# Performance work log

Measured on AMD Instinct MI355X. Metric: run time of the kernel, lower is better.

Reference implementation:

```python
import jax, jax.numpy as jnp
import numpy as np

B, S, DIN, DOUT = 2, 2048, 4096, 4096


def setup_inputs() -> dict:
    key = jax.random.key(0)
    k1, k2, k3, k4, k5 = jax.random.split(key, 5)
    x = jax.random.normal(k1, (B, S, DIN), dtype=jnp.float32)
    # int8-range weights stored as int32 (faithful to q_int_weight.float() upcast)
    q_int_weight = jax.random.randint(k2, (DIN, DOUT), 0, 256, dtype=jnp.int32)
    scale = jax.random.uniform(k3, (1,), dtype=jnp.float32) * 0.01 + 0.001
    zero_point = jax.random.uniform(k4, (1,), dtype=jnp.float32) * 128.0
    bias = jax.random.normal(k5, (DOUT,), dtype=jnp.float32)
    return {"x": x, "q_int_weight": q_int_weight, "scale": scale,
            "zero_point": zero_point, "bias": bias}


def reference(x, q_int_weight, scale, zero_point, bias):
    # Dequantize: (q - zero_point) * scale, per-tensor affine. Stored [in, out].
    w = (q_int_weight.astype(jnp.float32) - zero_point) * scale  # [DIN, DOUT]
    # F.linear(x_flat, w.t(), bias) == x @ w + bias
    y = jnp.einsum('bsi,io->bso', x, w) + bias  # [B, S, DOUT]
    return y
```

## Files before the change

### kernel.cpp

```cpp
#include <hip/hip_runtime.h>
#include <cstdint>
#include <cstddef>

#define M_DIM 4096
#define N_DIM 4096
#define K_DIM 4096
#define BM 128
#define BN 128
#define BKB 128

typedef __attribute__((ext_vector_type(4))) int i32x4;

__device__ __forceinline__ void async_copy16(const void* g, void* l) {
  __builtin_amdgcn_global_load_lds(
      (const __attribute__((address_space(1))) void*)g,
      (__attribute__((address_space(3))) void*)l,
      16, 0, 0);
}

__global__ __launch_bounds__(256) void convert_x_kernel(
    const float* __restrict__ x, signed char* __restrict__ xi,
    float* __restrict__ sx, float* __restrict__ rs) {
  __shared__ float red[8];
  const int t = threadIdx.x;
  const size_t row = blockIdx.x;
  const float* xr = x + row * (size_t)K_DIM;

  float4 v[4];
  float amax = 0.f;
#pragma unroll
  for (int i = 0; i < 4; ++i) {
    v[i] = *(const float4*)(xr + (i * 256 + t) * 4);
    amax = fmaxf(amax, fmaxf(fmaxf(fabsf(v[i].x), fabsf(v[i].y)),
                             fmaxf(fabsf(v[i].z), fabsf(v[i].w))));
  }
#pragma unroll
  for (int o = 32; o > 0; o >>= 1)
    amax = fmaxf(amax, __shfl_down(amax, o, 64));
  if ((t & 63) == 0) red[t >> 6] = amax;
  __syncthreads();
  amax = fmaxf(fmaxf(fmaxf(red[0], red[1]), fmaxf(red[2], red[3])), 1e-20f);
  const float inv = 127.f / amax;

  int ssum = 0;
  signed char* out = xi + row * (size_t)K_DIM;
#pragma unroll
  for (int i = 0; i < 4; ++i) {
    const int ia = __float2int_rn(v[i].x * inv);
    const int ib = __float2int_rn(v[i].y * inv);
    const int ic = __float2int_rn(v[i].z * inv);
    const int id = __float2int_rn(v[i].w * inv);
    ssum += ia + ib + ic + id;
    const int pk =
        (ia & 255) | ((ib & 255) << 8) | ((ic & 255) << 16) | (id << 24);
    *(int*)(out + (i * 256 + t) * 4) = pk;
  }
  float fs = (float)ssum;
#pragma unroll
  for (int o = 32; o > 0; o >>= 1) fs += __shfl_down(fs, o, 64);
  if ((t & 63) == 0) red[4 + (t >> 6)] = fs;
  __syncthreads();
  if (t == 0) {
    rs[row] = red[4] + red[5] + red[6] + red[7];
    sx[row] = amax * (1.f / 127.f);
  }
}

__global__ __launch_bounds__(256) void convert_w_kernel(
    const int* __restrict__ q, signed char* __restrict__ qsT) {
  __shared__ __align__(16) int qtile[64][68];
  const int t = threadIdx.x;
  const int k0 = (blockIdx.x & 63) << 6;
  const int n0 = (blockIdx.x >> 6) << 6;

  {
    const int c = t & 15;
    const int r0 = t >> 4;
#pragma unroll
    for (int i = 0; i < 4; ++i) {
      const int r = r0 + i * 16;
      const int4 v = *(const int4*)(q + (size_t)(k0 + r) * N_DIM + n0 + c * 4);
      *(int4*)&qtile[r][c * 4] = v;
    }
  }
  __syncthreads();
  {
    const int kc = t & 15;
    const int g = t >> 4;
    int4 v[4];
#pragma unroll
    for (int i = 0; i < 4; ++i) v[i] = *(const int4*)&qtile[kc * 4 + i][g * 4];
#pragma unroll
    for (int j = 0; j < 4; ++j) {
      const int b0 = ((&v[0].x)[j] - 128) & 255;
      const int b1 = ((&v[1].x)[j] - 128) & 255;
      const int b2 = ((&v[2].x)[j] - 128) & 255;
      const int b3 = ((&v[3].x)[j] - 128) & 255;
      const int pk = b0 | (b1 << 8) | (b2 << 16) | (b3 << 24);
      *(int*)(qsT + (size_t)(n0 + g * 4 + j) * K_DIM + k0 + kc * 4) = pk;
    }
  }
}

__global__ __launch_bounds__(256) void gemm_kernel(
    const signed char* __restrict__ A,
    const signed char* __restrict__ Bt,
    const float* __restrict__ bias, const float* __restrict__ sx,
    const float* __restrict__ rs, const float* __restrict__ scale_p,
    const float* __restrict__ zp_p, float* __restrict__ C) {
  __shared__ __align__(16) signed char As[BM * BKB];
  __shared__ __align__(16) signed char Bs[BN * BKB];

  const int tid = threadIdx.x;
  const int wave = tid >> 6;
  const int lane = tid & 63;
  const int wm = wave & 1;
  const int wn = wave >> 1;

  const int bm = blockIdx.x & 31;
  const int bn = blockIdx.x >> 5;
  const size_t m0 = (size_t)bm * BM;
  const size_t n0 = (size_t)bn * BN;

  const int srow = lane >> 3;
  const int schunk = (lane & 7) ^ (lane >> 3);

  const int quad = lane >> 4;
  const int lrow = lane & 15;
  const int rsw = lrow & 7;

  i32x4 acc[4][4];
  const i32x4 zero = {0, 0, 0, 0};
#pragma unroll
  for (int i = 0; i < 4; ++i)
#pragma unroll
    for (int j = 0; j < 4; ++j) acc[i][j] = zero;

  const signed char* Abase = A + m0 * K_DIM;
  const signed char* Bbase = Bt + n0 * K_DIM;

  for (int k0 = 0; k0 < K_DIM; k0 += BKB) {
#pragma unroll
    for (int j = 0; j < 4; ++j) {
      const int rbase = wave * 32 + j * 8;
      const int row = rbase + srow;
      const size_t goff = (size_t)row * K_DIM + k0 + schunk * 16;
      async_copy16(Abase + goff, As + rbase * BKB);
      async_copy16(Bbase + goff, Bs + rbase * BKB);
    }
    __syncthreads();

#pragma unroll
    for (int kh = 0; kh < 2; ++kh) {
      i32x4 af[4], bfr[4];
#pragma unroll
      for (int t = 0; t < 4; ++t) {
        const int ar = wm * 64 + t * 16 + lrow;
        const int br = wn * 64 + t * 16 + lrow;
        const int ch = (kh * 4 + quad) ^ rsw;
        af[t] = *(const i32x4*)(As + ar * BKB + ch * 16);
        bfr[t] = *(const i32x4*)(Bs + br * BKB + ch * 16);
      }
#pragma unroll
      for (int i = 0; i < 4; ++i)
#pragma unroll
        for (int j = 0; j < 4; ++j)
          acc[i][j] = __builtin_amdgcn_mfma_i32_16x16x64_i8(
              af[i], bfr[j], acc[i][j], 0, 0, 0);
    }
    __syncthreads();
  }

  const float scale = scale_p[0];
  const float c1 = 128.f - zp_p[0];
  float am[4][4], bm_[4][4];
#pragma unroll
  for (int i = 0; i < 4; ++i) {
    const size_t mbase = m0 + wm * 64 + i * 16 + quad * 4;
#pragma unroll
    for (int r = 0; r < 4; ++r) {
      const float a = scale * sx[mbase + r];
      am[i][r] = a;
      bm_[i][r] = a * c1 * rs[mbase + r];
    }
  }
#pragma unroll
  for (int j = 0; j < 4; ++j) {
    const size_t n = n0 + wn * 64 + j * 16 + lrow;
    const float bv = bias[n];
#pragma unroll
    for (int i = 0; i < 4; ++i) {
      const size_t mbase = m0 + wm * 64 + i * 16 + quad * 4;
#pragma unroll
      for (int r = 0; r < 4; ++r) {
        C[(mbase + r) * N_DIM + n] =
            fmaf(am[i][r], (float)acc[i][j][r], bm_[i][r] + bv);
      }
    }
  }
}

extern "C" void kernel_launch(void* const* d_in, const int* in_sizes, int n_in,
                              void* d_out, int out_size, void* d_ws,
                              size_t ws_size, hipStream_t stream) {
  const float* x = (const float*)d_in[0];
  const int* q = (const int*)d_in[1];
  const float* scale = (const float*)d_in[2];
  const float* zp = (const float*)d_in[3];
  const float* bias = (const float*)d_in[4];
  float* out = (float*)d_out;

  char* ws = (char*)d_ws;
  signed char* xi = (signed char*)ws;
  signed char* qsT = (signed char*)(ws + ((size_t)16 << 20));
  float* sx = (float*)(ws + ((size_t)32 << 20));
  float* rs = (float*)(ws + ((size_t)32 << 20) + (16 << 10));

  convert_x_kernel<<<4096, 256, 0, stream>>>(x, xi, sx, rs);
  convert_w_kernel<<<4096, 256, 0, stream>>>(q, qsT);
  gemm_kernel<<<1024, 256, 0, stream>>>(xi, qsT, bias, sx, rs, scale, zp, out);
}
```

Measured before the change: 262.0 us.

## Use 256x256 double-buffered int8 GEMM tiles with interleaved LDS loads and MFMA

Grows the GEMM block tile to 256x256 with 8 waves and double-buffers the A and B tiles in LDS, so the next K tile is loaded while the current one is multiplied. LDS fragment reads and MFMA groups are interleaved across barriers, with s_setprio raising priority during the MFMA groups. Blocks are remapped in a swizzled order to improve L2 reuse. The larger tile cuts global traffic per MFMA, but it uses 128KB of LDS and many accumulator registers. That limits occupancy, and 256 blocks leave only one wave of work across the device.

```diff
diff --git a/kernel.cpp b/kernel.cpp
--- a/kernel.cpp
+++ b/kernel.cpp
@@ -5,9 +5,10 @@
 #define M_DIM 4096
 #define N_DIM 4096
 #define K_DIM 4096
-#define BM 128
-#define BN 128
+#define BM 256
+#define BN 256
 #define BKB 128
+#define KTILES (K_DIM / BKB)
 
 typedef __attribute__((ext_vector_type(4))) int i32x4;
 
@@ -102,99 +103,149 @@
   }
 }
 
-__global__ __launch_bounds__(256) void gemm_kernel(
+__global__ __launch_bounds__(512, 2) void gemm_kernel(
     const signed char* __restrict__ A,
     const signed char* __restrict__ Bt,
     const float* __restrict__ bias, const float* __restrict__ sx,
     const float* __restrict__ rs, const float* __restrict__ scale_p,
     const float* __restrict__ zp_p, float* __restrict__ C) {
-  __shared__ __align__(16) signed char As[BM * BKB];
-  __shared__ __align__(16) signed char Bs[BN * BKB];
+  __shared__ __align__(16) signed char As[2][BM * BKB];
+  __shared__ __align__(16) signed char Bs[2][BN * BKB];
 
   const int tid = threadIdx.x;
   const int wave = tid >> 6;
   const int lane = tid & 63;
-  const int wm = wave & 1;
-  const int wn = wave >> 1;
-
-  const int bm = blockIdx.x & 31;
-  const int bn = blockIdx.x >> 5;
+  const int wm = wave >> 2;
+  const int wn = wave & 3;
+
+  const int swz = (blockIdx.x & 7) * 32 + (blockIdx.x >> 3);
+  const int bm = swz & 15;
+  const int bn = swz >> 4;
   const size_t m0 = (size_t)bm * BM;
   const size_t n0 = (size_t)bn * BN;
 
   const int srow = lane >> 3;
-  const int schunk = (lane & 7) ^ (lane >> 3);
+  const int schunk = (lane & 7) ^ srow;
 
   const int quad = lane >> 4;
   const int lrow = lane & 15;
   const int rsw = lrow & 7;
 
-  i32x4 acc[4][4];
+  const signed char* Abase = A + m0 * K_DIM + schunk * 16;
+  const signed char* Bbase = Bt + n0 * K_DIM + schunk * 16;
+
+  i32x4 acc[8][4];
   const i32x4 zero = {0, 0, 0, 0};
 #pragma unroll
-  for (int i = 0; i < 4; ++i)
+  for (int i = 0; i < 8; ++i)
 #pragma unroll
     for (int j = 0; j < 4; ++j) acc[i][j] = zero;
 
-  const signed char* Abase = A + m0 * K_DIM;
-  const signed char* Bbase = Bt + n0 * K_DIM;
-
-  for (int k0 = 0; k0 < K_DIM; k0 += BKB) {
+  auto stage = [&](int b, int k0) {
 #pragma unroll
     for (int j = 0; j < 4; ++j) {
-      const int rbase = wave * 32 + j * 8;
-      const int row = rbase + srow;
-      const size_t goff = (size_t)row * K_DIM + k0 + schunk * 16;
-      async_copy16(Abase + goff, As + rbase * BKB);
-      async_copy16(Bbase + goff, Bs + rbase * BKB);
-    }
-    __syncthreads();
-
-#pragma unroll
-    for (int kh = 0; kh < 2; ++kh) {
-      i32x4 af[4], bfr[4];
-#pragma unroll
-      for (int t = 0; t < 4; ++t) {
-        const int ar = wm * 64 + t * 16 + lrow;
-        const int br = wn * 64 + t * 16 + lrow;
-        const int ch = (kh * 4 + quad) ^ rsw;
-        af[t] = *(const i32x4*)(As + ar * BKB + ch * 16);
-        bfr[t] = *(const i32x4*)(Bs + br * BKB + ch * 16);
-      }
-#pragma unroll
-      for (int i = 0; i < 4; ++i)
-#pragma unroll
-        for (int j = 0; j < 4; ++j)
-          acc[i][j] = __builtin_amdgcn_mfma_i32_16x16x64_i8(
-              af[i], bfr[j], acc[i][j], 0, 0, 0);
-    }
-    __syncthreads();
-  }
+      const int rbase = j * 64 + wave * 8;
+      const size_t go = (size_t)(rbase + srow) * K_DIM + k0;
+      async_copy16(Abase + go, (void*)&As[b][rbase * BKB]);
+      async_copy16(Bbase + go, (void*)&Bs[b][rbase * BKB]);
+    }
+  };
+
+#define LDA(ig)                                                              \
+  do {                                                                       \
+    _Pragma("unroll") for (int kh = 0; kh < 2; ++kh)                         \
+        _Pragma("unroll") for (int t = 0; t < 4; ++t) {                      \
+      const int ar = wm * 128 + (ig) * 64 + t * 16 + lrow;                   \
+      av[kh][t] =                                                            \
+          *(const i32x4*)(as + ar * BKB + ((((kh << 2) | quad) ^ rsw) << 4));\
+    }                                                                        \
+  } while (0)
+
+#define LDB(jg)                                                              \
+  do {                                                                       \
+    _Pragma("unroll") for (int kh = 0; kh < 2; ++kh)                         \
+        _Pragma("unroll") for (int t = 0; t < 2; ++t) {                      \
+      const int br = wn * 64 + ((jg) * 2 + t) * 16 + lrow;                   \
+      bv[kh][(jg) * 2 + t] =                                                 \
+          *(const i32x4*)(bs + br * BKB + ((((kh << 2) | quad) ^ rsw) << 4));\
+    }                                                                        \
+  } while (0)
+
+#define MFMA16(ibase, j0)                                                    \
+  do {                                                                       \
+    __builtin_amdgcn_s_setprio(1);                                           \
+    _Pragma("unroll") for (int kh = 0; kh < 2; ++kh)                         \
+        _Pragma("unroll") for (int t = 0; t < 4; ++t)                        \
+            _Pragma("unroll") for (int j = 0; j < 2; ++j)                    \
+        acc[(ibase) + t][(j0) + j] = __builtin_amdgcn_mfma_i32_16x16x64_i8(  \
+            av[kh][t], bv[kh][(j0) + j], acc[(ibase) + t][(j0) + j], 0, 0,   \
+            0);                                                              \
+    __builtin_amdgcn_s_setprio(0);                                           \
+  } while (0)
+
+  stage(0, 0);
+  asm volatile("s_waitcnt vmcnt(0)" ::: "memory");
+  __builtin_amdgcn_s_barrier();
+
+#pragma unroll 2
+  for (int kt = 0; kt < KTILES; ++kt) {
+    const int buf = kt & 1;
+    const signed char* as = As[buf];
+    const signed char* bs = Bs[buf];
+
+    if (kt + 1 < KTILES) stage(buf ^ 1, (kt + 1) * BKB);
+
+    i32x4 av[2][4], bv[2][4];
+
+    LDA(0);
+    LDB(0);
+    __builtin_amdgcn_s_barrier();
+    MFMA16(0, 0);
+    __builtin_amdgcn_s_barrier();
+
+    LDB(1);
+    __builtin_amdgcn_s_barrier();
+    MFMA16(0, 2);
+    __builtin_amdgcn_s_barrier();
+
+    LDA(1);
+    __builtin_amdgcn_s_barrier();
+    MFMA16(4, 2);
+    __builtin_amdgcn_s_barrier();
+
+    MFMA16(4, 0);
+
+    __builtin_amdgcn_sched_barrier(0);
+    asm volatile("s_waitcnt lgkmcnt(0)" ::: "memory");
+    asm volatile("s_waitcnt vmcnt(0)" ::: "memory");
+    __builtin_amdgcn_sched_barrier(0);
+    __builtin_amdgcn_s_barrier();
+  }
+
+#undef LDA
+#undef LDB
+#undef MFMA16
 
   const float scale = scale_p[0];
   const float c1 = 128.f - zp_p[0];
-  float am[4][4], bm_[4][4];
-#pragma unroll
-  for (int i = 0; i < 4; ++i) {
-    const size_t mbase = m0 + wm * 64 + i * 16 + quad * 4;
+#pragma unroll
+  for (int i = 0; i < 8; ++i) {
+    const size_t mbase = m0 + wm * 128 + i * 16 + quad * 4;
+    float am[4], bmv[4];
 #pragma unroll
     for (int r = 0; r < 4; ++r) {
       const float a = scale * sx[mbase + r];
-      am[i][r] = a;
-      bm_[i][r] = a * c1 * rs[mbase + r];
-    }
-  }
-#pragma unroll
-  for (int j = 0; j < 4; ++j) {
-    const size_t n = n0 + wn * 64 + j * 16 + lrow;
-    const float bv = bias[n];
-#pragma unroll
-    for (int i = 0; i < 4; ++i) {
-      const size_t mbase = m0 + wm * 64 + i * 16 + quad * 4;
+      am[r] = a;
+      bmv[r] = a * c1 * rs[mbase + r];
+    }
+#pragma unroll
+    for (int j = 0; j < 4; ++j) {
+      const size_t n = n0 + wn * 64 + j * 16 + lrow;
+      const float bv = bias[n];
 #pragma unroll
       for (int r = 0; r < 4; ++r) {
         C[(mbase + r) * N_DIM + n] =
-            fmaf(am[i][r], (float)acc[i][j][r], bm_[i][r] + bv);
+            fmaf(am[r], (float)acc[i][j][r], bmv[r] + bv);
       }
     }
   }
@@ -218,5 +269,5 @@
 
   convert_x_kernel<<<4096, 256, 0, stream>>>(x, xi, sx, rs);
   convert_w_kernel<<<4096, 256, 0, stream>>>(q, qsT);
-  gemm_kernel<<<1024, 256, 0, stream>>>(xi, qsT, bias, sx, rs, scale, zp, out);
-}
+  gemm_kernel<<<256, 512, 0, stream>>>(xi, qsT, bias, sx, rs, scale, zp, out);
+}
```

Result: no change. 257.8 us (-1.6%).
